# Kernel tuning notes

Measured on AMD Instinct MI355X. Metric: run time of the kernel, lower is better.

Reference implementation:

```python
import jax, jax.numpy as jnp
import numpy as np
import math

NH, NR, HD, QK, ITERS = 8, 8, 64, 32, 4


def _pe(seq_len, dim):
    n = 1.0 / (1.0 + math.exp(-1))
    pos = np.arange(seq_len, dtype=np.float64)[:, None]
    i = np.arange(0, dim, 2, dtype=np.float64)[None, :]
    pe = np.zeros((seq_len, dim), np.float32)
    pe[:, 0::2] = n * np.sin(pos / 10000 ** (2 * i / dim))
    pe[:, 1::2] = n * np.cos(pos / 10000 ** (2 * (i + 1) / dim))
    return jnp.asarray(pe)


def _ln(x, g, b, eps=1e-5):
    m = x.mean(-1, keepdims=True)
    v = ((x - m) ** 2).mean(-1, keepdims=True)
    return (x - m) * jax.lax.rsqrt(v + eps) * g + b


def _comp_attn(x, norm1_g, norm1_b, norm2_g, norm2_b, q_w, q_b, k_w, k_b,
               v_w, v_b, qv_w, qv_b, score_w, score_b, final_w, final_b,
               ffn1_w, ffn1_b, ffn2_w, ffn2_b):
    B, S, D = x.shape
    res = x
    h = _ln(x, norm1_g, norm1_b)
    q = (h @ q_w + q_b).reshape(B, S, NH, HD).transpose(0, 2, 1, 3) / math.sqrt(HD)  # [B,nh,S,hd]
    k = (h @ k_w + k_b).reshape(B, S, NH, HD)                                         # [B,S,nh,hd]
    v = (h @ v_w + v_b).reshape(B, S, NR, HD)                                         # [B,S,nr,hd]
    score = jax.nn.softmax(jnp.einsum('bhqd,bkhd->bhqk', q, k), axis=-1)              # [B,nh,S,S]
    out = jnp.einsum('bhqk,bkrd->bqhrd', score, v)                                    # [B,S,nh,nr,hd]
    qv = (h @ qv_w + qv_b).reshape(B, S, NH, QK)
    qv_e = jnp.broadcast_to(qv[:, :, :, None, :], (B, S, NH, NR, QK))
    in_ = jnp.concatenate([qv_e, out], axis=-1)                                       # [B,S,nh,nr,qk+hd]
    comp = jax.nn.softmax(in_ @ score_w + score_b, axis=3)                            # [B,S,nh,nr,1]
    o = (comp * out).sum(axis=3).reshape(B, S, D)
    o = o @ final_w + final_b
    x = res + o
    res2 = x
    h2 = _ln(x, norm2_g, norm2_b)
    ff = jax.nn.relu(h2 @ ffn1_w + ffn1_b) @ ffn2_w + ffn2_b  # dropout identity (eval)
    return res2 + ff


def reference(img, qst, conv_w, conv_b, qrep_w, qrep_b, cls_token, map_w, map_b,
              norm1_g, norm1_b, norm2_g, norm2_b, q_w, q_b, k_w, k_b, v_w, v_b,
              qv_w, qv_b, score_w, score_b, final_w, final_b,
              ffn1_w, ffn1_b, ffn2_w, ffn2_b, out_w, out_b):
    B = img.shape[0]
    H = conv_w.shape[0]  # 256
    pe = _pe(25, H)
    # patch embedding: conv 15x15 stride 15 -> [B,H,5,5]
    p = jax.lax.conv_general_dilated(img, conv_w, (15, 15), 'VALID',
                                     dimension_numbers=('NCHW', 'OIHW', 'NCHW'))
    p = p + conv_b[None, :, None, None]
    p = p.reshape(B, H, 25).transpose(0, 2, 1) + pe[None]       # [B,25,H]
    cls = jnp.broadcast_to(cls_token, (B, 1, H))
    emb = jnp.concatenate([cls, p], axis=1)                      # [B,26,H]
    que = (qst @ qrep_w + qrep_b)[:, None, :]
    que = jnp.broadcast_to(que, (B, 26, H))
    x = jnp.concatenate([emb, que], axis=-1)                     # [B,26,2H]
    x = x @ map_w + map_b                                        # [B,26,D]
    for _ in range(ITERS):
        x = _comp_attn(x, norm1_g, norm1_b, norm2_g, norm2_b, q_w, q_b, k_w, k_b,
                       v_w, v_b, qv_w, qv_b, score_w, score_b, final_w, final_b,
                       ffn1_w, ffn1_b, ffn2_w, ffn2_b)
    y = x[:, 0, :] @ out_w + out_b
    return jax.nn.log_softmax(y, axis=1)


def setup_inputs() -> dict:
    key = jax.random.key(0)
    ks = iter(jax.random.split(key, 64))
    def rn(shape, s=0.02):
        return jax.random.normal(next(ks), shape, jnp.float32) * s
    B, D, H = 256, 512, 256
    return {
        'img': jax.random.normal(next(ks), (B, 3, 75, 75), jnp.float32),
        'qst': jax.random.normal(next(ks), (B, 18), jnp.float32),
        'conv_w': rn((H, 3, 15, 15)), 'conv_b': rn((H,)),
        'qrep_w': rn((18, H)), 'qrep_b': rn((H,)),
        'cls_token': rn((1, 1, H), 1.0),
        'map_w': rn((2 * H, D)), 'map_b': rn((D,)),
        'norm1_g': jnp.ones((D,), jnp.float32), 'norm1_b': jnp.zeros((D,), jnp.float32),
        'norm2_g': jnp.ones((D,), jnp.float32), 'norm2_b': jnp.zeros((D,), jnp.float32),
        'q_w': rn((D, D)), 'q_b': rn((D,)),
        'k_w': rn((D, D)), 'k_b': rn((D,)),
        'v_w': rn((D, NR * HD)), 'v_b': rn((NR * HD,)),
        'qv_w': rn((D, QK * NH)), 'qv_b': rn((QK * NH,)),
        'score_w': rn((HD + QK, 1)), 'score_b': rn((1,)),
        'final_w': rn((D, D)), 'final_b': rn((D,)),
        'ffn1_w': rn((D, 2 * D)), 'ffn1_b': rn((2 * D,)),
        'ffn2_w': rn((2 * D, D)), 'ffn2_b': rn((D,)),
        'out_w': rn((D, 10)), 'out_b': rn((10,)),
    }
```

## Files before the change

### kernel.cpp

```cpp
#include <hip/hip_runtime.h>
#include <math.h>

#define NB 256
#define SEQ 26
#define TOK (NB*SEQ)
#define DIM 512

typedef unsigned short u16;
typedef __attribute__((ext_vector_type(8))) short short8_t;
typedef __attribute__((ext_vector_type(4))) float floatx4;

__device__ inline u16 f2bf(float f) {
    union { float f; unsigned u; } v; v.f = f;
    unsigned r = v.u + 0x7fffu + ((v.u >> 16) & 1u);
    return (u16)(r >> 16);
}
__device__ inline float bf2f(u16 u) {
    union { unsigned u; float f; } v; v.u = ((unsigned)u) << 16; return v.f;
}

__device__ __forceinline__ void gload_lds16(const u16* g, u16* l) {
    __builtin_amdgcn_global_load_lds((const __attribute__((address_space(1))) void*)g,
                                     (__attribute__((address_space(3))) void*)l, 16, 0, 0);
}

__global__ void prep_all(const float* __restrict__ q_w, const float* __restrict__ k_w,
                         const float* __restrict__ v_w, const float* __restrict__ final_w,
                         const float* __restrict__ ffn1_w, const float* __restrict__ ffn2_w,
                         const float* __restrict__ map_w, const float* __restrict__ conv_w,
                         const float* __restrict__ q_b, const float* __restrict__ k_b,
                         const float* __restrict__ v_b, const float* __restrict__ cls,
                         u16* __restrict__ qkvT, u16* __restrict__ finT,
                         u16* __restrict__ f1T, u16* __restrict__ f2T,
                         u16* __restrict__ mapT, u16* __restrict__ cwT,
                         float* __restrict__ qkvb, u16* __restrict__ emb) {
    __shared__ float lds[64][65];
    int blk = blockIdx.x;
    int t = threadIdx.x;
    if (blk < 544) {
        const float* W; u16* Wt; int K, N, tbase;
        if (blk < 64)       { W = q_w;     Wt = qkvT;            K = 512;  N = 512;  tbase = 0;   }
        else if (blk < 128) { W = k_w;     Wt = qkvT + 512*512;  K = 512;  N = 512;  tbase = 64;  }
        else if (blk < 192) { W = v_w;     Wt = qkvT + 1024*512; K = 512;  N = 512;  tbase = 128; }
        else if (blk < 256) { W = final_w; Wt = finT;            K = 512;  N = 512;  tbase = 192; }
        else if (blk < 384) { W = ffn1_w;  Wt = f1T;             K = 512;  N = 1024; tbase = 256; }
        else if (blk < 512) { W = ffn2_w;  Wt = f2T;             K = 1024; N = 512;  tbase = 384; }
        else                { W = map_w;   Wt = mapT;            K = 256;  N = 512;  tbase = 512; }
        int tloc = blk - tbase;
        int ntn = N >> 6;
        int n0 = (tloc % ntn) * 64, k0 = (tloc / ntn) * 64;
        int j = t & 63, i0 = t >> 6;
        #pragma unroll
        for (int p = 0; p < 16; ++p) {
            int i = i0*16 + p;
            lds[i][j] = W[(size_t)(k0+i)*N + n0 + j];
        }
        __syncthreads();
        int i2 = t & 63, j0 = t >> 6;
        #pragma unroll
        for (int p = 0; p < 16; ++p) {
            int j2 = j0*16 + p;
            Wt[(size_t)(n0+j2)*K + k0 + i2] = f2bf(lds[i2][j2]);
        }
    } else if (blk < 544 + 256) {
        int oc = blk - 544;
        for (int jj = t; jj < 704; jj += 256)
            cwT[(size_t)oc*704 + jj] = (jj < 675) ? f2bf(conv_w[(size_t)oc*675 + jj]) : (u16)0;
    } else if (blk < 544 + 256 + 256) {
        int b = blk - 800;
        emb[(size_t)(b*SEQ)*256 + t] = f2bf(cls[t]);
    } else {
        for (int jj = t; jj < 1536; jj += 256)
            qkvb[jj] = jj < 512 ? q_b[jj] : (jj < 1024 ? k_b[jj-512] : v_b[jj-1024]);
    }
}

__global__ void im2col_kernel(const float* __restrict__ img, u16* __restrict__ P) {
    int ri = blockIdx.x;
    int b = ri / 25, pos = ri % 25, ph = pos/5, pw = pos%5;
    for (int j = threadIdx.x; j < 704; j += 256) {
        float v = 0.f;
        if (j < 675) {
            int c = j / 225, rem = j % 225, kh = rem/15, kw = rem%15;
            v = img[(size_t)((b*3+c)*75 + ph*15 + kh)*75 + pw*15 + kw];
        }
        P[(size_t)ri*704 + j] = f2bf(v);
    }
}

template<int RESMODE, int RELU, int OUTBF>
__global__ __launch_bounds__(512) void mfma_gemm(const u16* __restrict__ A, const u16* __restrict__ Bt,
                          const float* __restrict__ bias, const float* __restrict__ res,
                          void* __restrict__ Cout, int M, int N, int K, float alpha) {
    __shared__ __align__(16) u16 As[2][128*64];
    __shared__ __align__(16) u16 Bs[2][128*64];
    const int tid = threadIdx.x;
    const int lane = tid & 63;
    const int w = tid >> 6;
    const int wr = (w >> 2) * 64;
    const int wc = (w & 3) * 32;
    const int bm = blockIdx.y * 128, bn = blockIdx.x * 128;

    floatx4 acc[4][2];
    #pragma unroll
    for (int mi = 0; mi < 4; ++mi)
        #pragma unroll
        for (int ni = 0; ni < 2; ++ni)
            acc[mi][ni] = (floatx4){0.f,0.f,0.f,0.f};

    int idx0 = tid, idx1 = 512 + tid;
    int row0 = idx0 >> 3, ch0 = (idx0 & 7) ^ (row0 & 7);
    int row1 = idx1 >> 3, ch1 = (idx1 & 7) ^ (row1 & 7);
    const u16* a0 = &A [(size_t)(bm+row0)*K + ch0*8];
    const u16* a1 = &A [(size_t)(bm+row1)*K + ch1*8];
    const u16* b0 = &Bt[(size_t)(bn+row0)*K + ch0*8];
    const u16* b1 = &Bt[(size_t)(bn+row1)*K + ch1*8];

    const int nt = K >> 6;
    gload_lds16(a0, &As[0][idx0*8]);
    gload_lds16(a1, &As[0][idx1*8]);
    gload_lds16(b0, &Bs[0][idx0*8]);
    gload_lds16(b1, &Bs[0][idx1*8]);
    __syncthreads();

    for (int t = 0; t < nt; ++t) {
        const int cur = t & 1;
        if (t + 1 < nt) {
            int off = (t + 1) << 6;
            gload_lds16(a0 + off, &As[cur^1][idx0*8]);
            gload_lds16(a1 + off, &As[cur^1][idx1*8]);
            gload_lds16(b0 + off, &Bs[cur^1][idx0*8]);
            gload_lds16(b1 + off, &Bs[cur^1][idx1*8]);
        }
        #pragma unroll
        for (int kk = 0; kk < 2; ++kk) {
            int ch2 = kk*4 + (lane >> 4);
            short8_t af[4], bf[2];
            #pragma unroll
            for (int mi = 0; mi < 4; ++mi) {
                int row = wr + mi*16 + (lane & 15);
                af[mi] = *(const short8_t*)&As[cur][row*64 + ((ch2 ^ (row & 7))*8)];
            }
            #pragma unroll
            for (int ni = 0; ni < 2; ++ni) {
                int rowb = wc + ni*16 + (lane & 15);
                bf[ni] = *(const short8_t*)&Bs[cur][rowb*64 + ((ch2 ^ (rowb & 7))*8)];
            }
            #pragma unroll
            for (int mi = 0; mi < 4; ++mi)
                #pragma unroll
                for (int ni = 0; ni < 2; ++ni)
                    acc[mi][ni] = __builtin_amdgcn_mfma_f32_16x16x32_bf16(
                        af[mi], bf[ni], acc[mi][ni], 0, 0, 0);
        }
        __syncthreads();
    }

    #pragma unroll
    for (int mi = 0; mi < 4; ++mi) {
        #pragma unroll
        for (int ni = 0; ni < 2; ++ni) {
            int col = bn + wc + ni*16 + (lane & 15);
            float bv = bias ? bias[col] : 0.0f;
            #pragma unroll
            for (int r = 0; r < 4; ++r) {
                int row = bm + wr + mi*16 + (lane >> 4)*4 + r;
                float v = (acc[mi][ni][r] + bv) * alpha;
                if (RELU) v = fmaxf(v, 0.f);
                if (RESMODE == 1)      v += res[(size_t)row*N + col];
                else if (RESMODE == 2) v += res[(size_t)(row/SEQ)*N + col];
                if (RESMODE == 3) {
                    int bb = row / 25, pos = row - bb*25;
                    float freq = __powf(10000.0f, -(float)col / 128.0f);
                    float a = (float)pos * freq;
                    float pe = 0.7310585786300049f * ((col & 1) ? __cosf(a) : __sinf(a));
                    ((u16*)Cout)[(size_t)(bb*SEQ + 1 + pos)*256 + col] = f2bf(v + pe);
                } else if (OUTBF) {
                    ((u16*)Cout)[(size_t)row*N + col] = f2bf(v);
                } else {
                    ((float*)Cout)[(size_t)row*N + col] = v;
                }
            }
        }
    }
}

__global__ void que_map_kernel(const float* __restrict__ qst,
                               const float* __restrict__ qrep_w,
                               const float* __restrict__ qrep_b,
                               const float* __restrict__ map_w,
                               const float* __restrict__ map_b,
                               float* __restrict__ quem) {
    int b = blockIdx.x;
    int t = threadIdx.x;
    __shared__ float que[256];
    float acc = qrep_b[t];
    for (int j = 0; j < 18; ++j) acc += qst[b*18 + j] * qrep_w[j*256 + t];
    que[t] = acc;
    __syncthreads();
    for (int n = t; n < DIM; n += 256) {
        float a2 = map_b[n];
        for (int k = 0; k < 256; ++k) a2 += que[k] * map_w[(256 + k)*DIM + n];
        quem[b*DIM + n] = a2;
    }
}

__global__ void ln_kernel(const float* __restrict__ x, const float* __restrict__ g,
                          const float* __restrict__ bta, u16* __restrict__ out) {
    int t = blockIdx.x;
    int tid = threadIdx.x;
    const float* xr = x + (size_t)t*DIM;
    float v0 = xr[tid], v1 = xr[tid+256];
    float s = v0 + v1, sq = v0*v0 + v1*v1;
    __shared__ float rs[4], rq[4];
    for (int off = 32; off; off >>= 1) { s += __shfl_down(s, off); sq += __shfl_down(sq, off); }
    int wid = tid >> 6, lane = tid & 63;
    if (lane == 0) { rs[wid] = s; rq[wid] = sq; }
    __syncthreads();
    __shared__ float mean_s, rstd_s;
    if (tid == 0) {
        float ts = rs[0]+rs[1]+rs[2]+rs[3], tq = rq[0]+rq[1]+rq[2]+rq[3];
        float m = ts / DIM;
        float var = tq / DIM - m*m;
        mean_s = m; rstd_s = rsqrtf(var + 1e-5f);
    }
    __syncthreads();
    float m = mean_s, r = rstd_s;
    out[(size_t)t*DIM + tid]       = f2bf((v0 - m)*r*g[tid]     + bta[tid]);
    out[(size_t)t*DIM + tid + 256] = f2bf((v1 - m)*r*g[tid+256] + bta[tid+256]);
}

__global__ __launch_bounds__(512) void attn_fused_kernel(const u16* __restrict__ qkv,
                                                         const float* __restrict__ score_w,
                                                         u16* __restrict__ attn_o) {
    int b = blockIdx.x;
    __shared__ u16 Bt[64*224];
    __shared__ float s_lds[208*28];
    __shared__ float vwl[208];
    __shared__ float cmp_lds[208*8];
    __shared__ float swl[64];
    int tid = threadIdx.x;
    int lane = tid & 63, w = tid >> 6;

    if (tid < 64) swl[tid] = score_w[32 + tid];
    for (int k = 0; k < 26; ++k) {
        int d2 = tid & 63, r = tid >> 6;
        u16 v = qkv[(size_t)(b*SEQ+k)*1536 + 1024 + tid];
        int bo = (d2*448 + (k*8+r)*2) ^ ((d2 & 7) << 4);
        *(u16*)((char*)Bt + bo) = v;
    }
    {
        int d2 = tid & 63, kr = 208 + (tid >> 6);
        int bo1 = (d2*448 + kr*2)     ^ ((d2 & 7) << 4);
        int bo2 = (d2*448 + (kr+8)*2) ^ ((d2 & 7) << 4);
        *(u16*)((char*)Bt + bo1) = 0;
        *(u16*)((char*)Bt + bo2) = 0;
    }
    for (int row = tid; row < 208; row += 512) {
        s_lds[row*28 + 26] = 0.f; s_lds[row*28 + 27] = 0.f;
    }

    {
        int h = w;
        int col16 = lane & 15, ch = lane >> 4;
        short8_t qf[2][2], kf[2][2];
        #pragma unroll
        for (int mi = 0; mi < 2; ++mi) {
            int q = mi*16 + col16;
            #pragma unroll
            for (int kk = 0; kk < 2; ++kk) {
                if (q < 26)
                    qf[mi][kk] = *(const short8_t*)&qkv[(size_t)(b*SEQ+q)*1536 + h*64 + kk*32 + ch*8];
                else
                    qf[mi][kk] = (short8_t){0,0,0,0,0,0,0,0};
            }
        }
        #pragma unroll
        for (int ni = 0; ni < 2; ++ni) {
            int kq = ni*16 + col16;
            #pragma unroll
            for (int kk = 0; kk < 2; ++kk) {
                if (kq < 26)
                    kf[ni][kk] = *(const short8_t*)&qkv[(size_t)(b*SEQ+kq)*1536 + 512 + h*64 + kk*32 + ch*8];
                else
                    kf[ni][kk] = (short8_t){0,0,0,0,0,0,0,0};
            }
        }
        floatx4 sacc[2][2];
        #pragma unroll
        for (int mi = 0; mi < 2; ++mi)
            #pragma unroll
            for (int ni = 0; ni < 2; ++ni)
                sacc[mi][ni] = (floatx4){0.f,0.f,0.f,0.f};
        #pragma unroll
        for (int kk = 0; kk < 2; ++kk)
            #pragma unroll
            for (int mi = 0; mi < 2; ++mi)
                #pragma unroll
                for (int ni = 0; ni < 2; ++ni)
                    sacc[mi][ni] = __builtin_amdgcn_mfma_f32_16x16x32_bf16(
                        qf[mi][kk], kf[ni][kk], sacc[mi][ni], 0, 0, 0);
        #pragma unroll
        for (int mi = 0; mi < 2; ++mi) {
            #pragma unroll
            for (int r = 0; r < 4; ++r) {
                float s0 = sacc[mi][0][r] * 0.125f;
                float s1 = (col16 < 10) ? sacc[mi][1][r] * 0.125f : -1e30f;
                float mx = fmaxf(s0, s1);
                #pragma unroll
                for (int msk = 1; msk < 16; msk <<= 1) mx = fmaxf(mx, __shfl_xor(mx, msk));
                float e0 = __expf(s0 - mx);
                float e1 = (col16 < 10) ? __expf(s1 - mx) : 0.f;
                float den = e0 + e1;
                #pragma unroll
                for (int msk = 1; msk < 16; msk <<= 1) den += __shfl_xor(den, msk);
                float inv = 1.f / den;
                int q = mi*16 + ch*4 + r;
                if (q < 26) {
                    s_lds[(h*26+q)*28 + col16] = e0 * inv;
                    if (col16 < 10) s_lds[(h*26+q)*28 + 16 + col16] = e1 * inv;
                }
            }
        }
    }
    __syncthreads();

    if (tid < 208) {
        float acc = 0.f;
        for (int d2 = 0; d2 < 64; ++d2) {
            int bo = (d2*448 + tid*2) ^ ((d2 & 7) << 4);
            acc += bf2f(*(const u16*)((const char*)Bt + bo)) * swl[d2];
        }
        vwl[tid] = acc;
    }
    __syncthreads();

    if (tid < 208) {
        float srow[26];
        #pragma unroll
        for (int k = 0; k < 26; ++k) srow[k] = s_lds[tid*28 + k];
        float e[8];
        #pragma unroll
        for (int r = 0; r < 8; ++r) {
            float a = 0.f;
            #pragma unroll
            for (int k = 0; k < 26; ++k) a += srow[k] * vwl[k*8 + r];
            e[r] = a;
        }
        float m = e[0];
        #pragma unroll
        for (int r = 1; r < 8; ++r) m = fmaxf(m, e[r]);
        float den = 0.f;
        #pragma unroll
        for (int r = 0; r < 8; ++r) { e[r] = __expf(e[r]-m); den += e[r]; }
        float inv = 1.f/den;
        #pragma unroll
        for (int r = 0; r < 8; ++r) cmp_lds[tid*8+r] = e[r]*inv;
    }
    __syncthreads();

    int mh = w >> 2, nt = w & 3;
    int ntile0 = nt*16;
    short8_t bfr[7];
    #pragma unroll
    for (int ks = 0; ks < 7; ++ks) {
        int col = ntile0 + (lane & 15);
        int krb = ks*32 + (lane >> 4)*8;
        int bo = (col*448 + krb*2) ^ ((col & 7) << 4);
        bfr[ks] = *(const short8_t*)((const char*)Bt + bo);
    }
    int mt0 = mh ? 7 : 0, mt1 = mh ? 13 : 7;
    for (int mt = mt0; mt < mt1; ++mt) {
        int arow = mt*16 + (lane & 15);
        float c8[8];
        #pragma unroll
        for (int r = 0; r < 8; ++r) c8[r] = cmp_lds[arow*8 + r];
        floatx4 acc = (floatx4){0.f,0.f,0.f,0.f};
        #pragma unroll
        for (int ks = 0; ks < 7; ++ks) {
            int k = ks*4 + (lane >> 4);
            float sv = s_lds[arow*28 + k];
            short8_t af;
            #pragma unroll
            for (int j = 0; j < 8; ++j) af[j] = (short)f2bf(sv * c8[j]);
            acc = __builtin_amdgcn_mfma_f32_16x16x32_bf16(af, bfr[ks], acc, 0, 0, 0);
        }
        int colg = ntile0 + (lane & 15);
        #pragma unroll
        for (int rr = 0; rr < 4; ++rr) {
            int rowg = mt*16 + (lane >> 4)*4 + rr;
            int h = rowg / 26, q = rowg - h*26;
            attn_o[(size_t)(b*SEQ+q)*DIM + h*64 + colg] = f2bf(acc[rr]);
        }
    }
}

__global__ void head_kernel(const float* __restrict__ x, const float* __restrict__ out_w,
                            const float* __restrict__ out_b, float* __restrict__ y) {
    int b = blockIdx.x;
    int t = threadIdx.x;
    __shared__ float yv[10];
    if (t < 10) {
        float acc = out_b[t];
        const float* xr = x + (size_t)(b*SEQ)*DIM;
        for (int dd = 0; dd < DIM; ++dd) acc += xr[dd]*out_w[dd*10 + t];
        yv[t] = acc;
    }
    __syncthreads();
    if (t < 10) {
        float m = yv[0];
        for (int i = 1; i < 10; ++i) m = fmaxf(m, yv[i]);
        float den = 0.0f;
        for (int i = 0; i < 10; ++i) den += expf(yv[i]-m);
        y[b*10 + t] = yv[t] - m - logf(den);
    }
}

extern "C" void kernel_launch(void* const* d_in, const int* in_sizes, int n_in,
                              void* d_out, int out_size, void* d_ws, size_t ws_size,
                              hipStream_t stream) {
    const float* img      = (const float*)d_in[0];
    const float* qst      = (const float*)d_in[1];
    const float* conv_w   = (const float*)d_in[2];
    const float* conv_b   = (const float*)d_in[3];
    const float* qrep_w   = (const float*)d_in[4];
    const float* qrep_b   = (const float*)d_in[5];
    const float* cls_tok  = (const float*)d_in[6];
    const float* map_w    = (const float*)d_in[7];
    const float* map_b    = (const float*)d_in[8];
    const float* norm1_g  = (const float*)d_in[9];
    const float* norm1_b  = (const float*)d_in[10];
    const float* norm2_g  = (const float*)d_in[11];
    const float* norm2_b  = (const float*)d_in[12];
    const float* q_w      = (const float*)d_in[13];
    const float* q_b      = (const float*)d_in[14];
    const float* k_w      = (const float*)d_in[15];
    const float* k_b      = (const float*)d_in[16];
    const float* v_w      = (const float*)d_in[17];
    const float* v_b      = (const float*)d_in[18];
    const float* score_w  = (const float*)d_in[21];
    const float* final_w  = (const float*)d_in[23];
    const float* final_b  = (const float*)d_in[24];
    const float* ffn1_w   = (const float*)d_in[25];
    const float* ffn1_b   = (const float*)d_in[26];
    const float* ffn2_w   = (const float*)d_in[27];
    const float* ffn2_b   = (const float*)d_in[28];
    const float* out_w    = (const float*)d_in[29];
    const float* out_b    = (const float*)d_in[30];

    float* ws = (float*)d_ws;
    size_t o = 0;
    float* x    = ws + o;       o += (size_t)TOK*DIM;
    u16* qkvT   = (u16*)(ws+o); o += (size_t)1536*512/2;
    u16* finT   = (u16*)(ws+o); o += (size_t)512*512/2;
    u16* f1T    = (u16*)(ws+o); o += (size_t)1024*512/2;
    u16* f2T    = (u16*)(ws+o); o += (size_t)512*1024/2;
    u16* mapT   = (u16*)(ws+o); o += (size_t)512*256/2;
    u16* cwT    = (u16*)(ws+o); o += (size_t)256*704/2;
    float* qkvb = ws + o;       o += 1536;
    float* r2   = ws + o;
    u16*  h_bf    = (u16*)r2;
    u16*  qkv_bf  = (u16*)(r2 + (size_t)TOK*DIM/2);
    u16*  attn_obf= (u16*)(r2 + (size_t)TOK*DIM/2 + (size_t)TOK*1536/2);
    u16*  ffbuf   = qkv_bf;
    u16*  Pbuf    = (u16*)r2;
    u16*  emb_bf  = (u16*)(r2 + (size_t)6400*704/2);
    float* quem   = r2 + (size_t)6400*704/2 + (size_t)TOK*256/2;

    prep_all<<<1057, 256, 0, stream>>>(q_w, k_w, v_w, final_w, ffn1_w, ffn2_w, map_w, conv_w,
                                       q_b, k_b, v_b, cls_tok,
                                       qkvT, finT, f1T, f2T, mapT, cwT, qkvb, emb_bf);

    im2col_kernel<<<6400, 256, 0, stream>>>(img, Pbuf);
    que_map_kernel<<<NB, 256, 0, stream>>>(qst, qrep_w, qrep_b, map_w, map_b, quem);
    mfma_gemm<3,0,1><<<dim3(2,50), dim3(512), 0, stream>>>(
        Pbuf, cwT, conv_b, nullptr, emb_bf, 6400, 256, 704, 1.0f);
    mfma_gemm<2,0,0><<<dim3(4,52), dim3(512), 0, stream>>>(
        emb_bf, mapT, nullptr, quem, x, TOK, 512, 256, 1.0f);

    for (int it = 0; it < 4; ++it) {
        ln_kernel<<<TOK, 256, 0, stream>>>(x, norm1_g, norm1_b, h_bf);
        mfma_gemm<0,0,1><<<dim3(12,52), dim3(512), 0, stream>>>(
            h_bf, qkvT, qkvb, nullptr, qkv_bf, TOK, 1536, 512, 1.0f);
        attn_fused_kernel<<<NB, 512, 0, stream>>>(qkv_bf, score_w, attn_obf);
        mfma_gemm<1,0,0><<<dim3(4,52), dim3(512), 0, stream>>>(
            attn_obf, finT, final_b, x, x, TOK, 512, 512, 1.0f);
        ln_kernel<<<TOK, 256, 0, stream>>>(x, norm2_g, norm2_b, h_bf);
        mfma_gemm<0,1,1><<<dim3(8,52), dim3(512), 0, stream>>>(
            h_bf, f1T, ffn1_b, nullptr, ffbuf, TOK, 1024, 512, 1.0f);
        mfma_gemm<1,0,0><<<dim3(4,52), dim3(512), 0, stream>>>(
            ffbuf, f2T, ffn2_b, x, x, TOK, 512, 1024, 1.0f);
    }

    head_kernel<<<NB, 64, 0, stream>>>(x, out_w, out_b, (float*)d_out);
}
```

Before: 584.9 us.

## Use 64-row GEMM tiles for narrow outputs, parallelize head and fold que_map into prep

Templates the MFMA GEMM on the M tile height and uses 64-row tiles for the N=256/512 GEMMs, doubling the block count to fill more CUs on small-grid launches. Folds the question-embedding mapping kernel into the prep kernel to save a launch. Splits the attention value-weight reduction across two threads per row with a shuffle, and rewrites the classifier head to use 256 threads with wave reductions instead of 10 serial threads. Smaller tiles reduce data reuse per block, so each block loads its B tile more often relative to the work it does.

Result: faster. 540.9 us (-7.5%).

```diff
diff --git a/kernel.cpp b/kernel.cpp
--- a/kernel.cpp
+++ b/kernel.cpp
@@ -30,11 +30,15 @@
                          const float* __restrict__ map_w, const float* __restrict__ conv_w,
                          const float* __restrict__ q_b, const float* __restrict__ k_b,
                          const float* __restrict__ v_b, const float* __restrict__ cls,
+                         const float* __restrict__ qst, const float* __restrict__ qrep_w,
+                         const float* __restrict__ qrep_b, const float* __restrict__ map_b,
                          u16* __restrict__ qkvT, u16* __restrict__ finT,
                          u16* __restrict__ f1T, u16* __restrict__ f2T,
                          u16* __restrict__ mapT, u16* __restrict__ cwT,
-                         float* __restrict__ qkvb, u16* __restrict__ emb) {
+                         float* __restrict__ qkvb, u16* __restrict__ emb,
+                         float* __restrict__ quem) {
     __shared__ float lds[64][65];
+    __shared__ float que[256];
     int blk = blockIdx.x;
     int t = threadIdx.x;
     if (blk < 544) {
@@ -62,16 +66,27 @@
             int j2 = j0*16 + p;
             Wt[(size_t)(n0+j2)*K + k0 + i2] = f2bf(lds[i2][j2]);
         }
-    } else if (blk < 544 + 256) {
+    } else if (blk < 800) {
         int oc = blk - 544;
         for (int jj = t; jj < 704; jj += 256)
             cwT[(size_t)oc*704 + jj] = (jj < 675) ? f2bf(conv_w[(size_t)oc*675 + jj]) : (u16)0;
-    } else if (blk < 544 + 256 + 256) {
+    } else if (blk < 1056) {
         int b = blk - 800;
         emb[(size_t)(b*SEQ)*256 + t] = f2bf(cls[t]);
-    } else {
+    } else if (blk == 1056) {
         for (int jj = t; jj < 1536; jj += 256)
             qkvb[jj] = jj < 512 ? q_b[jj] : (jj < 1024 ? k_b[jj-512] : v_b[jj-1024]);
+    } else {
+        int b = blk - 1057;
+        float acc = qrep_b[t];
+        for (int j = 0; j < 18; ++j) acc += qst[b*18 + j] * qrep_w[j*256 + t];
+        que[t] = acc;
+        __syncthreads();
+        for (int n = t; n < DIM; n += 256) {
+            float a2 = map_b[n];
+            for (int k = 0; k < 256; ++k) a2 += que[k] * map_w[(256 + k)*DIM + n];
+            quem[b*DIM + n] = a2;
+        }
     }
 }
 
@@ -88,56 +103,69 @@
     }
 }
 
-template<int RESMODE, int RELU, int OUTBF>
+template<int BM, int RESMODE, int RELU, int OUTBF>
 __global__ __launch_bounds__(512) void mfma_gemm(const u16* __restrict__ A, const u16* __restrict__ Bt,
                           const float* __restrict__ bias, const float* __restrict__ res,
                           void* __restrict__ Cout, int M, int N, int K, float alpha) {
-    __shared__ __align__(16) u16 As[2][128*64];
+    constexpr int MI  = BM / 32;
+    constexpr int ALD = BM / 64;
+    __shared__ __align__(16) u16 As[2][BM*64];
     __shared__ __align__(16) u16 Bs[2][128*64];
     const int tid = threadIdx.x;
     const int lane = tid & 63;
     const int w = tid >> 6;
-    const int wr = (w >> 2) * 64;
+    const int wr = (w >> 2) * (MI*16);
     const int wc = (w & 3) * 32;
-    const int bm = blockIdx.y * 128, bn = blockIdx.x * 128;
-
-    floatx4 acc[4][2];
-    #pragma unroll
-    for (int mi = 0; mi < 4; ++mi)
+    const int bm = blockIdx.y * BM, bn = blockIdx.x * 128;
+
+    floatx4 acc[MI][2];
+    #pragma unroll
+    for (int mi = 0; mi < MI; ++mi)
         #pragma unroll
         for (int ni = 0; ni < 2; ++ni)
             acc[mi][ni] = (floatx4){0.f,0.f,0.f,0.f};
 
-    int idx0 = tid, idx1 = 512 + tid;
-    int row0 = idx0 >> 3, ch0 = (idx0 & 7) ^ (row0 & 7);
-    int row1 = idx1 >> 3, ch1 = (idx1 & 7) ^ (row1 & 7);
-    const u16* a0 = &A [(size_t)(bm+row0)*K + ch0*8];
-    const u16* a1 = &A [(size_t)(bm+row1)*K + ch1*8];
-    const u16* b0 = &Bt[(size_t)(bn+row0)*K + ch0*8];
-    const u16* b1 = &Bt[(size_t)(bn+row1)*K + ch1*8];
+    const u16* aptr[ALD];
+    int aidx[ALD];
+    #pragma unroll
+    for (int s = 0; s < ALD; ++s) {
+        int idx = s*512 + tid;
+        int row = idx >> 3, ch = (idx & 7) ^ (row & 7);
+        aptr[s] = &A[(size_t)(bm+row)*K + ch*8];
+        aidx[s] = idx;
+    }
+    const u16* bptr[2];
+    int bidx[2];
+    #pragma unroll
+    for (int s = 0; s < 2; ++s) {
+        int idx = s*512 + tid;
+        int row = idx >> 3, ch = (idx & 7) ^ (row & 7);
+        bptr[s] = &Bt[(size_t)(bn+row)*K + ch*8];
+        bidx[s] = idx;
+    }
 
     const int nt = K >> 6;
-    gload_lds16(a0, &As[0][idx0*8]);
-    gload_lds16(a1, &As[0][idx1*8]);
-    gload_lds16(b0, &Bs[0][idx0*8]);
-    gload_lds16(b1, &Bs[0][idx1*8]);
+    #pragma unroll
+    for (int s = 0; s < ALD; ++s) gload_lds16(aptr[s], &As[0][aidx[s]*8]);
+    #pragma unroll
+    for (int s = 0; s < 2; ++s)   gload_lds16(bptr[s], &Bs[0][bidx[s]*8]);
     __syncthreads();
 
     for (int t = 0; t < nt; ++t) {
         const int cur = t & 1;
         if (t + 1 < nt) {
             int off = (t + 1) << 6;
-            gload_lds16(a0 + off, &As[cur^1][idx0*8]);
-            gload_lds16(a1 + off, &As[cur^1][idx1*8]);
-            gload_lds16(b0 + off, &Bs[cur^1][idx0*8]);
-            gload_lds16(b1 + off, &Bs[cur^1][idx1*8]);
+            #pragma unroll
+            for (int s = 0; s < ALD; ++s) gload_lds16(aptr[s] + off, &As[cur^1][aidx[s]*8]);
+            #pragma unroll
+            for (int s = 0; s < 2; ++s)   gload_lds16(bptr[s] + off, &Bs[cur^1][bidx[s]*8]);
         }
         #pragma unroll
         for (int kk = 0; kk < 2; ++kk) {
             int ch2 = kk*4 + (lane >> 4);
-            short8_t af[4], bf[2];
-            #pragma unroll
-            for (int mi = 0; mi < 4; ++mi) {
+            short8_t af[MI], bf[2];
+            #pragma unroll
+            for (int mi = 0; mi < MI; ++mi) {
                 int row = wr + mi*16 + (lane & 15);
                 af[mi] = *(const short8_t*)&As[cur][row*64 + ((ch2 ^ (row & 7))*8)];
             }
@@ -147,7 +175,7 @@
                 bf[ni] = *(const short8_t*)&Bs[cur][rowb*64 + ((ch2 ^ (rowb & 7))*8)];
             }
             #pragma unroll
-            for (int mi = 0; mi < 4; ++mi)
+            for (int mi = 0; mi < MI; ++mi)
                 #pragma unroll
                 for (int ni = 0; ni < 2; ++ni)
                     acc[mi][ni] = __builtin_amdgcn_mfma_f32_16x16x32_bf16(
@@ -157,7 +185,7 @@
     }
 
     #pragma unroll
-    for (int mi = 0; mi < 4; ++mi) {
+    for (int mi = 0; mi < MI; ++mi) {
         #pragma unroll
         for (int ni = 0; ni < 2; ++ni) {
             int col = bn + wc + ni*16 + (lane & 15);
@@ -185,26 +213,6 @@
     }
 }
 
-__global__ void que_map_kernel(const float* __restrict__ qst,
-                               const float* __restrict__ qrep_w,
-                               const float* __restrict__ qrep_b,
-                               const float* __restrict__ map_w,
-                               const float* __restrict__ map_b,
-                               float* __restrict__ quem) {
-    int b = blockIdx.x;
-    int t = threadIdx.x;
-    __shared__ float que[256];
-    float acc = qrep_b[t];
-    for (int j = 0; j < 18; ++j) acc += qst[b*18 + j] * qrep_w[j*256 + t];
-    que[t] = acc;
-    __syncthreads();
-    for (int n = t; n < DIM; n += 256) {
-        float a2 = map_b[n];
-        for (int k = 0; k < 256; ++k) a2 += que[k] * map_w[(256 + k)*DIM + n];
-        quem[b*DIM + n] = a2;
-    }
-}
-
 __global__ void ln_kernel(const float* __restrict__ x, const float* __restrict__ g,
                           const float* __restrict__ bta, u16* __restrict__ out) {
     int t = blockIdx.x;
@@ -325,13 +333,17 @@
     }
     __syncthreads();
 
-    if (tid < 208) {
+    if (tid < 416) {
+        int kr = tid >> 1, h0 = (tid & 1) * 32;
         float acc = 0.f;
-        for (int d2 = 0; d2 < 64; ++d2) {
-            int bo = (d2*448 + tid*2) ^ ((d2 & 7) << 4);
+        #pragma unroll
+        for (int dd = 0; dd < 32; ++dd) {
+            int d2 = h0 + dd;
+            int bo = (d2*448 + kr*2) ^ ((d2 & 7) << 4);
             acc += bf2f(*(const u16*)((const char*)Bt + bo)) * swl[d2];
         }
-        vwl[tid] = acc;
+        acc += __shfl_xor(acc, 1);
+        if ((tid & 1) == 0) vwl[kr] = acc;
     }
     __syncthreads();
 
@@ -398,21 +410,35 @@
 __global__ void head_kernel(const float* __restrict__ x, const float* __restrict__ out_w,
                             const float* __restrict__ out_b, float* __restrict__ y) {
     int b = blockIdx.x;
-    int t = threadIdx.x;
+    int tid = threadIdx.x;
+    const float* xr = x + (size_t)(b*SEQ)*DIM;
+    float x0 = xr[tid], x1 = xr[tid+256];
+    float part[10];
+    #pragma unroll
+    for (int c = 0; c < 10; ++c)
+        part[c] = x0*out_w[tid*10 + c] + x1*out_w[(tid+256)*10 + c];
+    #pragma unroll
+    for (int off = 32; off; off >>= 1)
+        #pragma unroll
+        for (int c = 0; c < 10; ++c) part[c] += __shfl_down(part[c], off);
+    __shared__ float red[4][10];
     __shared__ float yv[10];
-    if (t < 10) {
-        float acc = out_b[t];
-        const float* xr = x + (size_t)(b*SEQ)*DIM;
-        for (int dd = 0; dd < DIM; ++dd) acc += xr[dd]*out_w[dd*10 + t];
-        yv[t] = acc;
-    }
-    __syncthreads();
-    if (t < 10) {
+    int wid = tid >> 6, lane = tid & 63;
+    if (lane == 0)
+        #pragma unroll
+        for (int c = 0; c < 10; ++c) red[wid][c] = part[c];
+    __syncthreads();
+    if (tid < 10)
+        yv[tid] = out_b[tid] + red[0][tid] + red[1][tid] + red[2][tid] + red[3][tid];
+    __syncthreads();
+    if (tid < 10) {
         float m = yv[0];
+        #pragma unroll
         for (int i = 1; i < 10; ++i) m = fmaxf(m, yv[i]);
         float den = 0.0f;
-        for (int i = 0; i < 10; ++i) den += expf(yv[i]-m);
-        y[b*10 + t] = yv[t] - m - logf(den);
+        #pragma unroll
+        for (int i = 0; i < 10; ++i) den += __expf(yv[i]-m);
+        y[b*10 + tid] = yv[tid] - m - __logf(den);
     }
 }
 
@@ -467,30 +493,29 @@
     u16*  emb_bf  = (u16*)(r2 + (size_t)6400*704/2);
     float* quem   = r2 + (size_t)6400*704/2 + (size_t)TOK*256/2;
 
-    prep_all<<<1057, 256, 0, stream>>>(q_w, k_w, v_w, final_w, ffn1_w, ffn2_w, map_w, conv_w,
-                                       q_b, k_b, v_b, cls_tok,
-                                       qkvT, finT, f1T, f2T, mapT, cwT, qkvb, emb_bf);
+    prep_all<<<1313, 256, 0, stream>>>(q_w, k_w, v_w, final_w, ffn1_w, ffn2_w, map_w, conv_w,
+                                       q_b, k_b, v_b, cls_tok, qst, qrep_w, qrep_b, map_b,
+                                       qkvT, finT, f1T, f2T, mapT, cwT, qkvb, emb_bf, quem);
 
     im2col_kernel<<<6400, 256, 0, stream>>>(img, Pbuf);
-    que_map_kernel<<<NB, 256, 0, stream>>>(qst, qrep_w, qrep_b, map_w, map_b, quem);
-    mfma_gemm<3,0,1><<<dim3(2,50), dim3(512), 0, stream>>>(
+    mfma_gemm<64,3,0,1><<<dim3(2,100), dim3(512), 0, stream>>>(
         Pbuf, cwT, conv_b, nullptr, emb_bf, 6400, 256, 704, 1.0f);
-    mfma_gemm<2,0,0><<<dim3(4,52), dim3(512), 0, stream>>>(
+    mfma_gemm<64,2,0,0><<<dim3(4,104), dim3(512), 0, stream>>>(
         emb_bf, mapT, nullptr, quem, x, TOK, 512, 256, 1.0f);
 
     for (int it = 0; it < 4; ++it) {
         ln_kernel<<<TOK, 256, 0, stream>>>(x, norm1_g, norm1_b, h_bf);
-        mfma_gemm<0,0,1><<<dim3(12,52), dim3(512), 0, stream>>>(
+        mfma_gemm<128,0,0,1><<<dim3(12,52), dim3(512), 0, stream>>>(
             h_bf, qkvT, qkvb, nullptr, qkv_bf, TOK, 1536, 512, 1.0f);
         attn_fused_kernel<<<NB, 512, 0, stream>>>(qkv_bf, score_w, attn_obf);
-        mfma_gemm<1,0,0><<<dim3(4,52), dim3(512), 0, stream>>>(
+        mfma_gemm<64,1,0,0><<<dim3(4,104), dim3(512), 0, stream>>>(
             attn_obf, finT, final_b, x, x, TOK, 512, 512, 1.0f);
         ln_kernel<<<TOK, 256, 0, stream>>>(x, norm2_g, norm2_b, h_bf);
-        mfma_gemm<0,1,1><<<dim3(8,52), dim3(512), 0, stream>>>(
+        mfma_gemm<128,0,1,1><<<dim3(8,52), dim3(512), 0, stream>>>(
             h_bf, f1T, ffn1_b, nullptr, ffbuf, TOK, 1024, 512, 1.0f);
-        mfma_gemm<1,0,0><<<dim3(4,52), dim3(512), 0, stream>>>(
+        mfma_gemm<64,1,0,0><<<dim3(4,104), dim3(512), 0, stream>>>(
             ffbuf, f2T, ffn2_b, x, x, TOK, 512, 1024, 1.0f);
     }
 
-    head_kernel<<<NB, 64, 0, stream>>>(x, out_w, out_b, (float*)d_out);
-}
+    head_kernel<<<NB, 256, 0, stream>>>(x, out_w, out_b, (float*)d_out);
+}
```
